# Kernel optimization log

Hardware: AMD Instinct MI355X
Metric: run time of the kernel (lower is better)

## Reference

```python
import jax, jax.numpy as jnp
import numpy as np
import math

N_VOX = 262144      # number of active voxels (input == output coords, stride=1)
C_IN = 64
C_OUT = 64
K_VOL = 27          # kernel_size**3
P_PER_OFF = 65536   # neighbor pairs per kernel offset (uniform nbsizes)


def setup_inputs() -> dict:
    key = jax.random.key(0)
    k1, k2, k3, k4 = jax.random.split(key, 4)
    feat = jax.random.normal(k1, (N_VOX, C_IN), dtype=jnp.float32)
    # reset_parameters: uniform(-std, std), std = 1/sqrt(in_channels * kernel_volume)
    std = 1.0 / math.sqrt(C_IN * K_VOL)
    kernel = jax.random.uniform(k2, (K_VOL, C_IN, C_OUT), dtype=jnp.float32,
                                minval=-std, maxval=std)
    src_ids = jax.random.randint(k3, (K_VOL, P_PER_OFF), 0, N_VOX, dtype=jnp.int32)
    tgt_ids = jax.random.randint(k4, (K_VOL, P_PER_OFF), 0, N_VOX, dtype=jnp.int32)
    return {"feat": feat, "kernel": kernel, "src_ids": src_ids, "tgt_ids": tgt_ids}


def reference(feat, kernel, src_ids, tgt_ids):
    # Sparse 3D conv (non-transposed): for each kernel offset k,
    #   out[tgt] += feat[src] @ kernel[k]
    # Gather per offset: [K, P, C_in]
    gathered = feat[src_ids]
    # Per-offset GEMM: [K, P, C_out]
    prod = jnp.einsum('kpi,kio->kpo', gathered, kernel)
    # Scatter-add into output voxels: [N_out, C_out]
    out = jax.ops.segment_sum(prod.reshape(-1, C_OUT), tgt_ids.reshape(-1),
                              num_segments=N_VOX)
    return out
```

## Files before the change

kernel.cpp:

```cpp
#include <hip/hip_runtime.h>

#define N_VOX 262144
#define C 64
#define K_VOL 27
#define P 65536

#define BLOCK 256
#define WAVES 4
#define PAIRS_PER_WAVE 256
#define NBATCH 16
#define BLOCKS_PER_K (P / (PAIRS_PER_WAVE * WAVES))

typedef __attribute__((ext_vector_type(8))) short bf16x8;
typedef __attribute__((ext_vector_type(4))) float f32x4;

__device__ inline unsigned short cvt_bf16_rne(float x) {
    unsigned u = __builtin_bit_cast(unsigned, x);
    u += 0x7fff + ((u >> 16) & 1);
    return (unsigned short)(u >> 16);
}
__device__ inline float bf16f(unsigned short h) {
    unsigned u = (unsigned)h << 16;
    return __builtin_bit_cast(float, u);
}

__global__ __launch_bounds__(BLOCK) void conv_mfma(
    const float* __restrict__ feat,
    const float* __restrict__ kern,
    const int* __restrict__ src_ids,
    const int* __restrict__ tgt_ids,
    float* __restrict__ out)
{
    const int k    = blockIdx.y;
    const int wave = threadIdx.x >> 6;
    const int lane = threadIdx.x & 63;
    const int g    = lane >> 4;
    const int col  = lane & 15;

    bf16x8 Bhi[2][4], Blo[2][4];
    {
        const float* Wk = kern + (size_t)k * C * C;
        #pragma unroll
        for (int kt = 0; kt < 2; ++kt)
            #pragma unroll
            for (int nt = 0; nt < 4; ++nt)
                #pragma unroll
                for (int i = 0; i < 8; ++i) {
                    float w = Wk[(size_t)(kt * 32 + g * 8 + i) * C + nt * 16 + col];
                    unsigned short h = cvt_bf16_rne(w);
                    Bhi[kt][nt][i] = (short)h;
                    Blo[kt][nt][i] = (short)cvt_bf16_rne(w - bf16f(h));
                }
    }

    const int pb0 = (blockIdx.x * WAVES + wave) * PAIRS_PER_WAVE;
    const int* srcp = src_ids + (size_t)k * P + pb0;
    const int* tgtp = tgt_ids + (size_t)k * P + pb0;

    f32x4 ra0, ra1, ra2, ra3;
    int tg0, tg1, tg2, tg3;

    int sv = srcp[col];
    {
        const float* fr = feat + (size_t)sv * C + g * 8;
        ra0 = *(const f32x4*)(fr);
        ra1 = *(const f32x4*)(fr + 4);
        ra2 = *(const f32x4*)(fr + 32);
        ra3 = *(const f32x4*)(fr + 36);
    }
    int sv_n = srcp[16 + col];
    tg0 = tgtp[g * 4 + 0];
    tg1 = tgtp[g * 4 + 1];
    tg2 = tgtp[g * 4 + 2];
    tg3 = tgtp[g * 4 + 3];

    for (int b = 0; b < NBATCH; ++b) {
        bf16x8 Ahi[2], Alo[2];
        #pragma unroll
        for (int i = 0; i < 4; ++i) {
            float x0 = ra0[i], x1 = ra1[i], x2 = ra2[i], x3 = ra3[i];
            unsigned short h;
            h = cvt_bf16_rne(x0); Ahi[0][i]     = (short)h; Alo[0][i]     = (short)cvt_bf16_rne(x0 - bf16f(h));
            h = cvt_bf16_rne(x1); Ahi[0][4 + i] = (short)h; Alo[0][4 + i] = (short)cvt_bf16_rne(x1 - bf16f(h));
            h = cvt_bf16_rne(x2); Ahi[1][i]     = (short)h; Alo[1][i]     = (short)cvt_bf16_rne(x2 - bf16f(h));
            h = cvt_bf16_rne(x3); Ahi[1][4 + i] = (short)h; Alo[1][4 + i] = (short)cvt_bf16_rne(x3 - bf16f(h));
        }

        const int ctg0 = tg0, ctg1 = tg1, ctg2 = tg2, ctg3 = tg3;
        if (b + 1 < NBATCH) {
            const int* tp = tgtp + (b + 1) * 16 + g * 4;
            tg0 = tp[0]; tg1 = tp[1]; tg2 = tp[2]; tg3 = tp[3];
        }

        if (b + 1 < NBATCH) {
            const float* fr = feat + (size_t)sv_n * C + g * 8;
            ra0 = *(const f32x4*)(fr);
            ra1 = *(const f32x4*)(fr + 4);
            ra2 = *(const f32x4*)(fr + 32);
            ra3 = *(const f32x4*)(fr + 36);
            if (b + 2 < NBATCH) sv_n = srcp[(b + 2) * 16 + col];
        }

        f32x4 acc[4] = {f32x4{0.f,0.f,0.f,0.f}, f32x4{0.f,0.f,0.f,0.f},
                        f32x4{0.f,0.f,0.f,0.f}, f32x4{0.f,0.f,0.f,0.f}};
        #pragma unroll
        for (int kt = 0; kt < 2; ++kt) {
            #pragma unroll
            for (int nt = 0; nt < 4; ++nt)
                acc[nt] = __builtin_amdgcn_mfma_f32_16x16x32_bf16(Ahi[kt], Bhi[kt][nt], acc[nt], 0, 0, 0);
            #pragma unroll
            for (int nt = 0; nt < 4; ++nt)
                acc[nt] = __builtin_amdgcn_mfma_f32_16x16x32_bf16(Alo[kt], Bhi[kt][nt], acc[nt], 0, 0, 0);
            #pragma unroll
            for (int nt = 0; nt < 4; ++nt)
                acc[nt] = __builtin_amdgcn_mfma_f32_16x16x32_bf16(Ahi[kt], Blo[kt][nt], acc[nt], 0, 0, 0);
        }

        float* o0 = out + (size_t)ctg0 * C + col;
        float* o1 = out + (size_t)ctg1 * C + col;
        float* o2 = out + (size_t)ctg2 * C + col;
        float* o3 = out + (size_t)ctg3 * C + col;
        #pragma unroll
        for (int nt = 0; nt < 4; ++nt) {
            unsafeAtomicAdd(o0 + nt * 16, acc[nt][0]);
            unsafeAtomicAdd(o1 + nt * 16, acc[nt][1]);
            unsafeAtomicAdd(o2 + nt * 16, acc[nt][2]);
            unsafeAtomicAdd(o3 + nt * 16, acc[nt][3]);
        }
    }
}

extern "C" void kernel_launch(void* const* d_in, const int* in_sizes, int n_in,
                              void* d_out, int out_size, void* d_ws, size_t ws_size,
                              hipStream_t stream)
{
    const float* feat = (const float*)d_in[0];
    const float* kern = (const float*)d_in[1];
    const int*   src  = (const int*)d_in[2];
    const int*   tgt  = (const int*)d_in[3];
    float* out = (float*)d_out;

    hipMemsetAsync(out, 0, (size_t)N_VOX * C * sizeof(float), stream);

    dim3 grid(BLOCKS_PER_K, K_VOL);
    conv_mfma<<<grid, BLOCK, 0, stream>>>(feat, kern, src, tgt, out);
}
```

Baseline: 470.7 us.

## Bin pairs by target row block and accumulate in LDS tiles

Adds a binning pass that buckets all (src, tgt, k) pairs by 256-row target block. A per-bin kernel then sorts the pairs by kernel offset in LDS, runs the split-bf16 MFMA GEMMs, and accumulates with LDS atomics before one coalesced write per bin. This replaces the scattered global float atomics and the output memset. Split weights are precomputed once, and an overflow path handles bins that exceed capacity. The cost is the extra binning pass with global atomics and a larger workspace; if the workspace is too small it falls back to the old kernel without prefetching.

```diff
diff --git a/kernel.cpp b/kernel.cpp
--- a/kernel.cpp
+++ b/kernel.cpp
@@ -4,12 +4,23 @@
 #define C 64
 #define K_VOL 27
 #define P 65536
-
-#define BLOCK 256
-#define WAVES 4
-#define PAIRS_PER_WAVE 256
-#define NBATCH 16
-#define BLOCKS_PER_K (P / (PAIRS_PER_WAVE * WAVES))
+#define NPAIR (K_VOL * P)
+
+#define BIN_ROWS 256
+#define NBINS (N_VOX / BIN_ROWS)
+#define CAP 2048
+#define REC_SLOTS 2464
+#define MAXG (REC_SLOTS / 16)
+
+#define W_SZ      (K_VOL * 2 * 4 * 64 * 16)
+#define W_HI_OFF  0
+#define W_LO_OFF  W_SZ
+#define CNT_OFF   (2 * W_SZ)
+#define OCNT_OFF  (CNT_OFF + NBINS * 4)
+#define OVF_CAP   4096
+#define OVF_OFF   (OCNT_OFF + 64)
+#define REC_OFF   (OVF_OFF + OVF_CAP * 8)
+#define WS_NEED   ((size_t)REC_OFF + (size_t)NBINS * CAP * 4)
 
 typedef __attribute__((ext_vector_type(8))) short bf16x8;
 typedef __attribute__((ext_vector_type(4))) float f32x4;
@@ -24,19 +35,213 @@
     return __builtin_bit_cast(float, u);
 }
 
-__global__ __launch_bounds__(BLOCK) void conv_mfma(
+__global__ void w_prep(const float* __restrict__ kern, unsigned char* __restrict__ ws) {
+    const int k = blockIdx.x, lane = threadIdx.x;
+    const int g4 = lane >> 4, col = lane & 15;
+    const float* Wk = kern + (size_t)k * C * C;
+    bf16x8* hi = (bf16x8*)(ws + W_HI_OFF);
+    bf16x8* lo = (bf16x8*)(ws + W_LO_OFF);
+    #pragma unroll
+    for (int kt = 0; kt < 2; ++kt)
+        #pragma unroll
+        for (int nt = 0; nt < 4; ++nt) {
+            bf16x8 h, l;
+            #pragma unroll
+            for (int i = 0; i < 8; ++i) {
+                float w = Wk[(size_t)(kt * 32 + g4 * 8 + i) * C + nt * 16 + col];
+                unsigned short hs = cvt_bf16_rne(w);
+                h[i] = (short)hs;
+                l[i] = (short)cvt_bf16_rne(w - bf16f(hs));
+            }
+            int idx = ((k * 2 + kt) * 4 + nt) * 64 + lane;
+            hi[idx] = h;
+            lo[idx] = l;
+        }
+}
+
+__global__ void binning(const int* __restrict__ src, const int* __restrict__ tgt,
+                        unsigned char* __restrict__ ws) {
+    unsigned* cnt  = (unsigned*)(ws + CNT_OFF);
+    unsigned* ocnt = (unsigned*)(ws + OCNT_OFF);
+    uint2*    ovf  = (uint2*)(ws + OVF_OFF);
+    unsigned* rec  = (unsigned*)(ws + REC_OFF);
+    for (int j = blockIdx.x * blockDim.x + threadIdx.x; j < NPAIR;
+         j += gridDim.x * blockDim.x) {
+        int k = j >> 16;
+        unsigned s = (unsigned)src[j];
+        unsigned t = (unsigned)tgt[j];
+        unsigned r = ((t & 255u) << 23) | ((unsigned)k << 18) | s;
+        unsigned bin = t >> 8;
+        unsigned pos = atomicAdd(&cnt[bin], 1u);
+        if (pos < CAP) rec[(size_t)bin * CAP + pos] = r;
+        else {
+            unsigned op = atomicAdd(ocnt, 1u);
+            if (op < OVF_CAP) ovf[op] = make_uint2(((unsigned)k << 18) | s, t);
+        }
+    }
+}
+
+__global__ __launch_bounds__(512, 4) void conv_bin(
     const float* __restrict__ feat,
-    const float* __restrict__ kern,
-    const int* __restrict__ src_ids,
-    const int* __restrict__ tgt_ids,
+    const unsigned char* __restrict__ ws,
     float* __restrict__ out)
 {
-    const int k    = blockIdx.y;
-    const int wave = threadIdx.x >> 6;
-    const int lane = threadIdx.x & 63;
-    const int g    = lane >> 4;
-    const int col  = lane & 15;
-
+    __shared__ float tile[(BIN_ROWS + 1) * C];
+    __shared__ unsigned srec[REC_SLOTS];
+    __shared__ unsigned khist[K_VOL], koff[K_VOL];
+    __shared__ unsigned short grp2k[MAXG + 2];
+    __shared__ unsigned sG;
+
+    const int bin  = blockIdx.x;
+    const int tid  = threadIdx.x;
+    const int wave = tid >> 6, lane = tid & 63;
+    const int g4 = lane >> 4, col = lane & 15;
+
+    const unsigned* cnt = (const unsigned*)(ws + CNT_OFF);
+    const unsigned* rec = (const unsigned*)(ws + REC_OFF) + (size_t)bin * CAP;
+    const unsigned nrec = min(cnt[bin], (unsigned)CAP);
+
+    for (int i = tid; i < (BIN_ROWS + 1) * C; i += 512) tile[i] = 0.f;
+    for (int i = tid; i < REC_SLOTS; i += 512) srec[i] = 0xFFFFFFFFu;
+    if (tid < K_VOL) khist[tid] = 0u;
+    __syncthreads();
+
+    for (unsigned i = tid; i < nrec; i += 512)
+        atomicAdd(&khist[(rec[i] >> 18) & 31u], 1u);
+    __syncthreads();
+
+    if (tid == 0) {
+        unsigned base = 0, g = 0;
+        for (int k = 0; k < K_VOL; ++k) {
+            koff[k] = base;
+            unsigned ng = (khist[k] + 15u) >> 4;
+            for (unsigned q = 0; q < ng; ++q) grp2k[g++] = (unsigned short)k;
+            base += ng << 4;
+        }
+        sG = g;
+    }
+    __syncthreads();
+    const unsigned G = sG;
+
+    for (unsigned i = tid; i < nrec; i += 512) {
+        unsigned r = rec[i];
+        unsigned pos = atomicAdd(&koff[(r >> 18) & 31u], 1u);
+        srec[pos] = r;
+    }
+    __syncthreads();
+
+    const bf16x8* whi = (const bf16x8*)(ws + W_HI_OFF);
+    const bf16x8* wlo = (const bf16x8*)(ws + W_LO_OFF);
+    const unsigned gs = (G * (unsigned)wave) >> 3;
+    const unsigned ge = (G * (unsigned)(wave + 1)) >> 3;
+
+    bf16x8 Bhi[2][4], Blo[2][4];
+    int curk = -1;
+
+    for (unsigned g = gs; g < ge; ++g) {
+        const int k = (int)grp2k[g];
+        if (k != curk) {
+            curk = k;
+            #pragma unroll
+            for (int kt = 0; kt < 2; ++kt)
+                #pragma unroll
+                for (int nt = 0; nt < 4; ++nt) {
+                    int idx = ((k * 2 + kt) * 4 + nt) * 64 + lane;
+                    Bhi[kt][nt] = whi[idx];
+                    Blo[kt][nt] = wlo[idx];
+                }
+        }
+
+        const unsigned rb = g * 16;
+        const unsigned myrec = srec[rb + col];
+        const unsigned q0 = srec[rb + g4 * 4 + 0];
+        const unsigned q1 = srec[rb + g4 * 4 + 1];
+        const unsigned q2 = srec[rb + g4 * 4 + 2];
+        const unsigned q3 = srec[rb + g4 * 4 + 3];
+        const int row0 = (q0 == 0xFFFFFFFFu) ? 256 : (int)((q0 >> 23) & 255u);
+        const int row1 = (q1 == 0xFFFFFFFFu) ? 256 : (int)((q1 >> 23) & 255u);
+        const int row2 = (q2 == 0xFFFFFFFFu) ? 256 : (int)((q2 >> 23) & 255u);
+        const int row3 = (q3 == 0xFFFFFFFFu) ? 256 : (int)((q3 >> 23) & 255u);
+
+        const float* fr = feat + (size_t)(myrec & 0x3FFFFu) * C + g4 * 8;
+        f32x4 ra0 = *(const f32x4*)(fr);
+        f32x4 ra1 = *(const f32x4*)(fr + 4);
+        f32x4 ra2 = *(const f32x4*)(fr + 32);
+        f32x4 ra3 = *(const f32x4*)(fr + 36);
+
+        bf16x8 Ahi[2], Alo[2];
+        #pragma unroll
+        for (int i = 0; i < 4; ++i) {
+            float x0 = ra0[i], x1 = ra1[i], x2 = ra2[i], x3 = ra3[i];
+            unsigned short h;
+            h = cvt_bf16_rne(x0); Ahi[0][i]     = (short)h; Alo[0][i]     = (short)cvt_bf16_rne(x0 - bf16f(h));
+            h = cvt_bf16_rne(x1); Ahi[0][4 + i] = (short)h; Alo[0][4 + i] = (short)cvt_bf16_rne(x1 - bf16f(h));
+            h = cvt_bf16_rne(x2); Ahi[1][i]     = (short)h; Alo[1][i]     = (short)cvt_bf16_rne(x2 - bf16f(h));
+            h = cvt_bf16_rne(x3); Ahi[1][4 + i] = (short)h; Alo[1][4 + i] = (short)cvt_bf16_rne(x3 - bf16f(h));
+        }
+
+        f32x4 acc[4] = {f32x4{0.f,0.f,0.f,0.f}, f32x4{0.f,0.f,0.f,0.f},
+                        f32x4{0.f,0.f,0.f,0.f}, f32x4{0.f,0.f,0.f,0.f}};
+        #pragma unroll
+        for (int kt = 0; kt < 2; ++kt) {
+            #pragma unroll
+            for (int nt = 0; nt < 4; ++nt)
+                acc[nt] = __builtin_amdgcn_mfma_f32_16x16x32_bf16(Ahi[kt], Bhi[kt][nt], acc[nt], 0, 0, 0);
+            #pragma unroll
+            for (int nt = 0; nt < 4; ++nt)
+                acc[nt] = __builtin_amdgcn_mfma_f32_16x16x32_bf16(Alo[kt], Bhi[kt][nt], acc[nt], 0, 0, 0);
+            #pragma unroll
+            for (int nt = 0; nt < 4; ++nt)
+                acc[nt] = __builtin_amdgcn_mfma_f32_16x16x32_bf16(Ahi[kt], Blo[kt][nt], acc[nt], 0, 0, 0);
+        }
+
+        float* t0 = &tile[row0 * C + col];
+        float* t1 = &tile[row1 * C + col];
+        float* t2 = &tile[row2 * C + col];
+        float* t3 = &tile[row3 * C + col];
+        #pragma unroll
+        for (int nt = 0; nt < 4; ++nt) {
+            atomicAdd(t0 + nt * 16, acc[nt][0]);
+            atomicAdd(t1 + nt * 16, acc[nt][1]);
+            atomicAdd(t2 + nt * 16, acc[nt][2]);
+            atomicAdd(t3 + nt * 16, acc[nt][3]);
+        }
+    }
+    __syncthreads();
+
+    float* ob = out + (size_t)bin * BIN_ROWS * C;
+    for (int i = tid * 4; i < BIN_ROWS * C; i += 512 * 4)
+        *(float4*)(ob + i) = *(const float4*)&tile[i];
+}
+
+__global__ void ovf_fix(const float* __restrict__ feat, const float* __restrict__ kern,
+                        const unsigned char* __restrict__ ws, float* __restrict__ out) {
+    const unsigned* ocnt = (const unsigned*)(ws + OCNT_OFF);
+    const uint2*    ovf  = (const uint2*)(ws + OVF_OFF);
+    const unsigned n = min(*ocnt, (unsigned)OVF_CAP);
+    const int ch = threadIdx.x & 63;
+    const unsigned r0 = (blockIdx.x * blockDim.x + threadIdx.x) >> 6;
+    const unsigned stride = (gridDim.x * blockDim.x) >> 6;
+    for (unsigned r = r0; r < n; r += stride) {
+        uint2 e = ovf[r];
+        unsigned s = e.x & 0x3FFFFu, k = (e.x >> 18) & 31u, t = e.y;
+        const float* fr = feat + (size_t)s * C;
+        const float* Wk = kern + (size_t)k * C * C + ch;
+        float a = 0.f;
+        for (int i = 0; i < C; ++i) a = fmaf(fr[i], Wk[(size_t)i * C], a);
+        unsafeAtomicAdd(out + (size_t)t * C + ch, a);
+    }
+}
+
+#define FB_PAIRS_PER_WAVE 256
+#define FB_NBATCH 16
+__global__ __launch_bounds__(256) void conv_mfma(
+    const float* __restrict__ feat, const float* __restrict__ kern,
+    const int* __restrict__ src_ids, const int* __restrict__ tgt_ids,
+    float* __restrict__ out)
+{
+    const int k = blockIdx.y, wave = threadIdx.x >> 6, lane = threadIdx.x & 63;
+    const int g = lane >> 4, col = lane & 15;
     bf16x8 Bhi[2][4], Blo[2][4];
     {
         const float* Wk = kern + (size_t)k * C * C;
@@ -52,29 +257,16 @@
                     Blo[kt][nt][i] = (short)cvt_bf16_rne(w - bf16f(h));
                 }
     }
-
-    const int pb0 = (blockIdx.x * WAVES + wave) * PAIRS_PER_WAVE;
+    const int pb0 = (blockIdx.x * 4 + wave) * FB_PAIRS_PER_WAVE;
     const int* srcp = src_ids + (size_t)k * P + pb0;
     const int* tgtp = tgt_ids + (size_t)k * P + pb0;
-
-    f32x4 ra0, ra1, ra2, ra3;
-    int tg0, tg1, tg2, tg3;
-
-    int sv = srcp[col];
-    {
+    for (int b = 0; b < FB_NBATCH; ++b) {
+        int sv = srcp[b * 16 + col];
         const float* fr = feat + (size_t)sv * C + g * 8;
-        ra0 = *(const f32x4*)(fr);
-        ra1 = *(const f32x4*)(fr + 4);
-        ra2 = *(const f32x4*)(fr + 32);
-        ra3 = *(const f32x4*)(fr + 36);
-    }
-    int sv_n = srcp[16 + col];
-    tg0 = tgtp[g * 4 + 0];
-    tg1 = tgtp[g * 4 + 1];
-    tg2 = tgtp[g * 4 + 2];
-    tg3 = tgtp[g * 4 + 3];
-
-    for (int b = 0; b < NBATCH; ++b) {
+        f32x4 ra0 = *(const f32x4*)(fr), ra1 = *(const f32x4*)(fr + 4);
+        f32x4 ra2 = *(const f32x4*)(fr + 32), ra3 = *(const f32x4*)(fr + 36);
+        int tg0 = tgtp[b * 16 + g * 4 + 0], tg1 = tgtp[b * 16 + g * 4 + 1];
+        int tg2 = tgtp[b * 16 + g * 4 + 2], tg3 = tgtp[b * 16 + g * 4 + 3];
         bf16x8 Ahi[2], Alo[2];
         #pragma unroll
         for (int i = 0; i < 4; ++i) {
@@ -85,22 +277,6 @@
             h = cvt_bf16_rne(x2); Ahi[1][i]     = (short)h; Alo[1][i]     = (short)cvt_bf16_rne(x2 - bf16f(h));
             h = cvt_bf16_rne(x3); Ahi[1][4 + i] = (short)h; Alo[1][4 + i] = (short)cvt_bf16_rne(x3 - bf16f(h));
         }
-
-        const int ctg0 = tg0, ctg1 = tg1, ctg2 = tg2, ctg3 = tg3;
-        if (b + 1 < NBATCH) {
-            const int* tp = tgtp + (b + 1) * 16 + g * 4;
-            tg0 = tp[0]; tg1 = tp[1]; tg2 = tp[2]; tg3 = tp[3];
-        }
-
-        if (b + 1 < NBATCH) {
-            const float* fr = feat + (size_t)sv_n * C + g * 8;
-            ra0 = *(const f32x4*)(fr);
-            ra1 = *(const f32x4*)(fr + 4);
-            ra2 = *(const f32x4*)(fr + 32);
-            ra3 = *(const f32x4*)(fr + 36);
-            if (b + 2 < NBATCH) sv_n = srcp[(b + 2) * 16 + col];
-        }
-
         f32x4 acc[4] = {f32x4{0.f,0.f,0.f,0.f}, f32x4{0.f,0.f,0.f,0.f},
                         f32x4{0.f,0.f,0.f,0.f}, f32x4{0.f,0.f,0.f,0.f}};
         #pragma unroll
@@ -115,11 +291,10 @@
             for (int nt = 0; nt < 4; ++nt)
                 acc[nt] = __builtin_amdgcn_mfma_f32_16x16x32_bf16(Ahi[kt], Blo[kt][nt], acc[nt], 0, 0, 0);
         }
-
-        float* o0 = out + (size_t)ctg0 * C + col;
-        float* o1 = out + (size_t)ctg1 * C + col;
-        float* o2 = out + (size_t)ctg2 * C + col;
-        float* o3 = out + (size_t)ctg3 * C + col;
+        float* o0 = out + (size_t)tg0 * C + col;
+        float* o1 = out + (size_t)tg1 * C + col;
+        float* o2 = out + (size_t)tg2 * C + col;
+        float* o3 = out + (size_t)tg3 * C + col;
         #pragma unroll
         for (int nt = 0; nt < 4; ++nt) {
             unsafeAtomicAdd(o0 + nt * 16, acc[nt][0]);
@@ -139,9 +314,17 @@
     const int*   src  = (const int*)d_in[2];
     const int*   tgt  = (const int*)d_in[3];
     float* out = (float*)d_out;
-
-    hipMemsetAsync(out, 0, (size_t)N_VOX * C * sizeof(float), stream);
-
-    dim3 grid(BLOCKS_PER_K, K_VOL);
-    conv_mfma<<<grid, BLOCK, 0, stream>>>(feat, kern, src, tgt, out);
-}
+    unsigned char* ws = (unsigned char*)d_ws;
+
+    if (ws_size >= WS_NEED) {
+        hipMemsetAsync(ws + CNT_OFF, 0, NBINS * 4 + 64, stream);
+        w_prep<<<K_VOL, 64, 0, stream>>>(kern, ws);
+        binning<<<2048, 256, 0, stream>>>(src, tgt, ws);
+        conv_bin<<<NBINS, 512, 0, stream>>>(feat, ws, out);
+        ovf_fix<<<16, 256, 0, stream>>>(feat, kern, ws, out);
+    } else {
+        hipMemsetAsync(out, 0, (size_t)N_VOX * C * sizeof(float), stream);
+        dim3 grid(P / (FB_PAIRS_PER_WAVE * 4), K_VOL);
+        conv_mfma<<<grid, 256, 0, stream>>>(feat, kern, src, tgt, out);
+    }
+}
```

Measured after the change: 1.127 ms. +139.5%, slower.
